# Kernel optimization log

Measured on AMD Instinct MI355X. Metric: run time of the kernel, lower is better.

Reference implementation:

```python
import jax, jax.numpy as jnp
import numpy as np

B, P, D, H = 2048, 128, 64, 8
DB = 10  # D_obs + D_pos = 7 + 3, hard-coded in the module


def setup_inputs() -> dict:
    key = jax.random.key(0)
    ks = jax.random.split(key, 10)
    s = lambda fan_in: 1.0 / np.sqrt(fan_in)
    return {
        "x": jax.random.normal(ks[0], (B, D), dtype=jnp.float32),
        "b": jax.random.normal(ks[1], (B, P, DB), dtype=jnp.float32),
        "W_kvx": jax.random.uniform(ks[2], (D, 2 * H * D), jnp.float32, -s(D), s(D)),
        "b_kvx": jax.random.uniform(ks[3], (2 * H * D,), jnp.float32, -s(D), s(D)),
        "W_kvb": jax.random.uniform(ks[4], (DB, 2 * H * D), jnp.float32, -s(DB), s(DB)),
        "b_kvb": jax.random.uniform(ks[5], (2 * H * D,), jnp.float32, -s(DB), s(DB)),
        "W_q": jax.random.uniform(ks[6], (D, H * D), jnp.float32, -s(D), s(D)),
        "b_q": jax.random.uniform(ks[7], (H * D,), jnp.float32, -s(D), s(D)),
        "W_f": jax.random.uniform(ks[8], (H * D, D), jnp.float32, -s(H * D), s(H * D)),
        "b_f": jax.random.uniform(ks[9], (D,), jnp.float32, -s(H * D), s(H * D)),
    }


def reference(x, b, W_kvx, b_kvx, W_kvb, b_kvb, W_q, b_q, W_f, b_f):
    Bn, Dx = x.shape
    _, Pn, _ = b.shape
    # dual projections + broadcast add: [B,1,2HD] + [B,P,2HD]
    kv = (x @ W_kvx + b_kvx)[:, None, :] + (jnp.einsum('bpe,ef->bpf', b, W_kvb) + b_kvb)
    k, v = jnp.split(kv, 2, axis=-1)            # each [B,P,H*D]
    k = k.reshape(Bn, Pn, H, Dx)
    v = v.reshape(Bn, Pn, H, Dx)
    q = (x @ W_q + b_q).reshape(Bn, H, Dx)
    dots = jnp.einsum('bphd,bhd->bph', k, q) / np.sqrt(Dx).astype(np.float32)
    # NOTE: faithful to source — softmax over the HEAD axis (last dim of [B,P,H])
    attn = jax.nn.softmax(dots, axis=-1)
    vals = jnp.einsum('bph,bphd->bhd', attn, v)  # sum over positions P
    out = vals.reshape(Bn, H * Dx) @ W_f + b_f
    return out
```

## Files before the change

### kernel.cpp

```cpp
#include <hip/hip_runtime.h>

#define NDB 10

__global__ __launch_bounds__(256) void proj_kernel(
    const float* __restrict__ x, const float* __restrict__ W_kvx,
    const float* __restrict__ b_kvx, const float* __restrict__ b_kvb,
    const float* __restrict__ W_q, const float* __restrict__ b_q,
    float* __restrict__ XQ)
{
    __shared__ float x_t[64][68];
    const int t = threadIdx.x;
    const int row0 = blockIdx.x * 64;
    const int ct = blockIdx.y;

    {
        const int r = t & 63, kb = (t >> 6) * 16;
        float4 xv[4];
        #pragma unroll
        for (int i = 0; i < 4; ++i)
            xv[i] = *(const float4*)&x[(size_t)(row0 + r) * 64 + kb + i * 4];
        #pragma unroll
        for (int i = 0; i < 4; ++i) {
            x_t[kb + i * 4 + 0][r] = xv[i].x;
            x_t[kb + i * 4 + 1][r] = xv[i].y;
            x_t[kb + i * 4 + 2][r] = xv[i].z;
            x_t[kb + i * 4 + 3][r] = xv[i].w;
        }
    }
    __syncthreads();

    const bool iskv = (ct < 16);
    const int c0 = (iskv ? ct * 64 : (ct - 16) * 64) + (t & 15) * 4;
    const int stride = iskv ? 1024 : 512;
    const float* Wp = (iskv ? W_kvx : W_q) + c0;
    const int r0 = (t >> 4) * 4;

    float acc[4][4] = {};
    #pragma unroll 8
    for (int k = 0; k < 64; ++k) {
        float4 a  = *(const float4*)&x_t[k][r0];
        float4 wv = *(const float4*)&Wp[k * stride];
        float av[4] = {a.x, a.y, a.z, a.w};
        float wvv[4] = {wv.x, wv.y, wv.z, wv.w};
        #pragma unroll
        for (int i = 0; i < 4; ++i)
            #pragma unroll
            for (int jj = 0; jj < 4; ++jj)
                acc[i][jj] = fmaf(av[i], wvv[jj], acc[i][jj]);
    }
    float4 bias;
    if (iskv) {
        float4 b1 = *(const float4*)&b_kvx[c0];
        float4 b2 = *(const float4*)&b_kvb[c0];
        bias.x = b1.x + b2.x; bias.y = b1.y + b2.y;
        bias.z = b1.z + b2.z; bias.w = b1.w + b2.w;
    } else {
        bias = *(const float4*)&b_q[c0];
    }
    const int outcol = ct * 64 + (t & 15) * 4;
    #pragma unroll
    for (int i = 0; i < 4; ++i) {
        float4 o;
        o.x = acc[i][0] + bias.x; o.y = acc[i][1] + bias.y;
        o.z = acc[i][2] + bias.z; o.w = acc[i][3] + bias.w;
        *(float4*)&XQ[(size_t)(row0 + r0 + i) * 1536 + outcol] = o;
    }
}

__global__ __launch_bounds__(256) void attn_core(
    const float* __restrict__ bmat, const float* __restrict__ W_kvb,
    const float* __restrict__ XQ, const float* __restrict__ W_f,
    const float* __restrict__ b_f, float* __restrict__ out)
{
    __shared__ float bb_s[128][11];
    __shared__ float q_s[8][68];
    __shared__ float dot0_s[8];
    __shared__ float Wqkb_s[NDB][8];
    __shared__ float partA[4][8];
    __shared__ float partS[4][NDB][8];
    __shared__ float A_s[8];
    __shared__ float S_s[NDB][8];
    __shared__ float vals_s[512];
    __shared__ float pout[4][64];

    const int t = threadIdx.x, lane = t & 63, w = t >> 6;
    const int row = blockIdx.x;
    const float* __restrict__ xq = XQ + (size_t)row * 1536;

    {
        const float* bsrc = bmat + (size_t)row * 1280;
        #pragma unroll
        for (int i = 0; i < 5; ++i) {
            int idx = t + 256 * i;
            bb_s[idx / 10][idx % 10] = bsrc[idx];
        }
        float qa = xq[1024 + t];
        float qb = xq[1024 + 256 + t];
        q_s[t >> 6][t & 63] = qa;
        q_s[(t + 256) >> 6][t & 63] = qb;
        float p1 = xq[t] * qa;
        float p2 = xq[t + 256] * qb;
        #pragma unroll
        for (int m = 1; m <= 32; m <<= 1) p1 += __shfl_xor(p1, m);
        #pragma unroll
        for (int m = 1; m <= 32; m <<= 1) p2 += __shfl_xor(p2, m);
        if (lane == 0) { dot0_s[w] = p1; dot0_s[w + 4] = p2; }
    }
    __syncthreads();

    {
        const int g = t >> 3, l = t & 7;
        #pragma unroll
        for (int ro = 0; ro < 3; ++ro) {
            int o = g + 32 * ro;
            if (o < 80) {
                int e = o >> 3, h = o & 7;
                float s = 0.f;
                #pragma unroll
                for (int m = 0; m < 8; ++m) {
                    int d = l + 8 * m;
                    s = fmaf(W_kvb[e * 1024 + h * 64 + d], q_s[h][d], s);
                }
                s += __shfl_xor(s, 1); s += __shfl_xor(s, 2); s += __shfl_xor(s, 4);
                if (l == 0) Wqkb_s[e][h] = s;
            }
        }
    }
    __syncthreads();

    {
        const int hh = lane & 7, pg = lane >> 3;
        float wq[NDB];
        #pragma unroll
        for (int e = 0; e < NDB; ++e) wq[e] = Wqkb_s[e][hh];
        const float d0v = dot0_s[hh];
        float aA = 0.f, aS[NDB];
        #pragma unroll
        for (int e = 0; e < NDB; ++e) aS[e] = 0.f;
        #pragma unroll
        for (int it = 0; it < 4; ++it) {
            int p = w * 32 + pg + 8 * it;
            float bbv[NDB];
            #pragma unroll
            for (int e = 0; e < NDB; ++e) bbv[e] = bb_s[p][e];
            float dot = d0v;
            #pragma unroll
            for (int e = 0; e < NDB; ++e) dot = fmaf(bbv[e], wq[e], dot);
            dot *= 0.125f;
            float m = dot;
            m = fmaxf(m, __shfl_xor(m, 1));
            m = fmaxf(m, __shfl_xor(m, 2));
            m = fmaxf(m, __shfl_xor(m, 4));
            float ex = __expf(dot - m);
            float sum = ex;
            sum += __shfl_xor(sum, 1); sum += __shfl_xor(sum, 2); sum += __shfl_xor(sum, 4);
            float at = ex * __builtin_amdgcn_rcpf(sum);
            aA += at;
            #pragma unroll
            for (int e = 0; e < NDB; ++e) aS[e] = fmaf(at, bbv[e], aS[e]);
        }
        aA += __shfl_xor(aA, 8); aA += __shfl_xor(aA, 16); aA += __shfl_xor(aA, 32);
        #pragma unroll
        for (int e = 0; e < NDB; ++e) {
            aS[e] += __shfl_xor(aS[e], 8);
            aS[e] += __shfl_xor(aS[e], 16);
            aS[e] += __shfl_xor(aS[e], 32);
        }
        if (pg == 0) {
            partA[w][hh] = aA;
            #pragma unroll
            for (int e = 0; e < NDB; ++e) partS[w][e][hh] = aS[e];
        }
    }
    __syncthreads();

    if (t < 8)  A_s[t] = partA[0][t] + partA[1][t] + partA[2][t] + partA[3][t];
    if (t < 80) {
        int e = t >> 3, h = t & 7;
        S_s[e][h] = partS[0][e][h] + partS[1][e][h] + partS[2][e][h] + partS[3][e][h];
    }
    __syncthreads();

    {
        int f1 = t, f2 = t + 256;
        float v1 = A_s[w] * xq[512 + f1];
        float v2 = A_s[w + 4] * xq[512 + f2];
        #pragma unroll
        for (int e = 0; e < NDB; ++e) {
            v1 = fmaf(S_s[e][w],     W_kvb[e * 1024 + 512 + f1], v1);
            v2 = fmaf(S_s[e][w + 4], W_kvb[e * 1024 + 512 + f2], v2);
        }
        vals_s[f1] = v1;
        vals_s[f2] = v2;
    }
    __syncthreads();

    {
        const int j = lane;
        float acc = 0.f;
        #pragma unroll 8
        for (int k4 = 0; k4 < 32; ++k4) {
            int f = w * 128 + k4 * 4;
            float4 v = *(const float4*)&vals_s[f];
            acc = fmaf(v.x, W_f[(f + 0) * 64 + j], acc);
            acc = fmaf(v.y, W_f[(f + 1) * 64 + j], acc);
            acc = fmaf(v.z, W_f[(f + 2) * 64 + j], acc);
            acc = fmaf(v.w, W_f[(f + 3) * 64 + j], acc);
        }
        pout[w][j] = acc;
    }
    __syncthreads();

    if (t < 64)
        out[(size_t)row * 64 + t] =
            pout[0][t] + pout[1][t] + pout[2][t] + pout[3][t] + b_f[t];
}

extern "C" void kernel_launch(void* const* d_in, const int* in_sizes, int n_in,
                              void* d_out, int out_size, void* d_ws, size_t ws_size,
                              hipStream_t stream)
{
    const float* x     = (const float*)d_in[0];
    const float* bmat  = (const float*)d_in[1];
    const float* W_kvx = (const float*)d_in[2];
    const float* b_kvx = (const float*)d_in[3];
    const float* W_kvb = (const float*)d_in[4];
    const float* b_kvb = (const float*)d_in[5];
    const float* W_q   = (const float*)d_in[6];
    const float* b_q   = (const float*)d_in[7];
    const float* W_f   = (const float*)d_in[8];
    const float* b_f   = (const float*)d_in[9];
    float* out = (float*)d_out;
    float* XQ  = (float*)d_ws;

    proj_kernel<<<dim3(32, 24), 256, 0, stream>>>(x, W_kvx, b_kvx, b_kvb, W_q, b_q, XQ);
    attn_core<<<2048, 256, 0, stream>>>(bmat, W_kvb, XQ, W_f, b_f, out);
}
```

Baseline: 109.2 us.

## Fold W_f into value projection weights to skip per-row output GEMV

```diff
diff --git a/kernel.cpp b/kernel.cpp
--- a/kernel.cpp
+++ b/kernel.cpp
@@ -1,12 +1,45 @@
 #include <hip/hip_runtime.h>
 
 #define NDB 10
+
+__global__ __launch_bounds__(256) void fold_kernel(
+    const float* __restrict__ W_kvx, const float* __restrict__ b_kvx,
+    const float* __restrict__ W_kvb, const float* __restrict__ b_kvb,
+    const float* __restrict__ W_f, float* __restrict__ M,
+    float* __restrict__ c, float* __restrict__ T)
+{
+    const int r = blockIdx.x;
+    const int col = blockIdx.y * 256 + threadIdx.x;
+    const int h = col >> 6, j = col & 63;
+
+    const float* wfp = W_f + (size_t)(h * 64) * 64 + j;
+    float acc = 0.f;
+    if (r < 64) {
+        const float* src = W_kvx + (size_t)r * 1024 + 512 + h * 64;
+        #pragma unroll 8
+        for (int d = 0; d < 64; ++d) acc = fmaf(src[d], wfp[d * 64], acc);
+        M[(size_t)r * 512 + col] = acc;
+    } else if (r < 74) {
+        const int e = r - 64;
+        const float* src = W_kvb + (size_t)e * 1024 + 512 + h * 64;
+        #pragma unroll 8
+        for (int d = 0; d < 64; ++d) acc = fmaf(src[d], wfp[d * 64], acc);
+        T[(size_t)e * 512 + col] = acc;
+    } else {
+        const float* s1 = b_kvx + 512 + h * 64;
+        const float* s2 = b_kvb + 512 + h * 64;
+        #pragma unroll 8
+        for (int d = 0; d < 64; ++d) acc = fmaf(s1[d] + s2[d], wfp[d * 64], acc);
+        c[col] = acc;
+    }
+}
 
 __global__ __launch_bounds__(256) void proj_kernel(
     const float* __restrict__ x, const float* __restrict__ W_kvx,
     const float* __restrict__ b_kvx, const float* __restrict__ b_kvb,
     const float* __restrict__ W_q, const float* __restrict__ b_q,
-    float* __restrict__ XQ)
+    const float* __restrict__ M, const float* __restrict__ c,
+    float* __restrict__ XU)
 {
     __shared__ float x_t[64][68];
     const int t = threadIdx.x;
@@ -29,10 +62,12 @@
     }
     __syncthreads();
 
-    const bool iskv = (ct < 16);
-    const int c0 = (iskv ? ct * 64 : (ct - 16) * 64) + (t & 15) * 4;
-    const int stride = iskv ? 1024 : 512;
-    const float* Wp = (iskv ? W_kvx : W_q) + c0;
+    const int cc = (t & 15) * 4;
+    const float* Wp; int stride, c0;
+    if (ct < 8)       { Wp = W_kvx; stride = 1024; c0 = ct * 64 + cc; }
+    else if (ct < 16) { Wp = W_q;   stride = 512;  c0 = (ct - 8) * 64 + cc; }
+    else              { Wp = M;     stride = 512;  c0 = (ct - 16) * 64 + cc; }
+    Wp += c0;
     const int r0 = (t >> 4) * 4;
 
     float acc[4][4] = {};
@@ -49,27 +84,29 @@
                 acc[i][jj] = fmaf(av[i], wvv[jj], acc[i][jj]);
     }
     float4 bias;
-    if (iskv) {
+    if (ct < 8) {
         float4 b1 = *(const float4*)&b_kvx[c0];
         float4 b2 = *(const float4*)&b_kvb[c0];
         bias.x = b1.x + b2.x; bias.y = b1.y + b2.y;
         bias.z = b1.z + b2.z; bias.w = b1.w + b2.w;
+    } else if (ct < 16) {
+        bias = *(const float4*)&b_q[c0];
     } else {
-        bias = *(const float4*)&b_q[c0];
-    }
-    const int outcol = ct * 64 + (t & 15) * 4;
+        bias = *(const float4*)&c[c0];
+    }
+    const int outcol = ct * 64 + cc;
     #pragma unroll
     for (int i = 0; i < 4; ++i) {
         float4 o;
         o.x = acc[i][0] + bias.x; o.y = acc[i][1] + bias.y;
         o.z = acc[i][2] + bias.z; o.w = acc[i][3] + bias.w;
-        *(float4*)&XQ[(size_t)(row0 + r0 + i) * 1536 + outcol] = o;
+        *(float4*)&XU[(size_t)(row0 + r0 + i) * 1536 + outcol] = o;
     }
 }
 
 __global__ __launch_bounds__(256) void attn_core(
     const float* __restrict__ bmat, const float* __restrict__ W_kvb,
-    const float* __restrict__ XQ, const float* __restrict__ W_f,
+    const float* __restrict__ XU, const float* __restrict__ T,
     const float* __restrict__ b_f, float* __restrict__ out)
 {
     __shared__ float bb_s[128][11];
@@ -80,12 +117,11 @@
     __shared__ float partS[4][NDB][8];
     __shared__ float A_s[8];
     __shared__ float S_s[NDB][8];
-    __shared__ float vals_s[512];
     __shared__ float pout[4][64];
 
     const int t = threadIdx.x, lane = t & 63, w = t >> 6;
     const int row = blockIdx.x;
-    const float* __restrict__ xq = XQ + (size_t)row * 1536;
+    const float* __restrict__ xq = XU + (size_t)row * 1536;
 
     {
         const float* bsrc = bmat + (size_t)row * 1280;
@@ -94,8 +130,8 @@
             int idx = t + 256 * i;
             bb_s[idx / 10][idx % 10] = bsrc[idx];
         }
-        float qa = xq[1024 + t];
-        float qb = xq[1024 + 256 + t];
+        float qa = xq[512 + t];
+        float qb = xq[512 + 256 + t];
         q_s[t >> 6][t & 63] = qa;
         q_s[(t + 256) >> 6][t & 63] = qb;
         float p1 = xq[t] * qa;
@@ -182,30 +218,15 @@
     __syncthreads();
 
     {
-        int f1 = t, f2 = t + 256;
-        float v1 = A_s[w] * xq[512 + f1];
-        float v2 = A_s[w + 4] * xq[512 + f2];
-        #pragma unroll
-        for (int e = 0; e < NDB; ++e) {
-            v1 = fmaf(S_s[e][w],     W_kvb[e * 1024 + 512 + f1], v1);
-            v2 = fmaf(S_s[e][w + 4], W_kvb[e * 1024 + 512 + f2], v2);
-        }
-        vals_s[f1] = v1;
-        vals_s[f2] = v2;
-    }
-    __syncthreads();
-
-    {
         const int j = lane;
         float acc = 0.f;
-        #pragma unroll 8
-        for (int k4 = 0; k4 < 32; ++k4) {
-            int f = w * 128 + k4 * 4;
-            float4 v = *(const float4*)&vals_s[f];
-            acc = fmaf(v.x, W_f[(f + 0) * 64 + j], acc);
-            acc = fmaf(v.y, W_f[(f + 1) * 64 + j], acc);
-            acc = fmaf(v.z, W_f[(f + 2) * 64 + j], acc);
-            acc = fmaf(v.w, W_f[(f + 3) * 64 + j], acc);
+        #pragma unroll
+        for (int hi = 0; hi < 2; ++hi) {
+            int h = 2 * w + hi;
+            acc = fmaf(A_s[h], xq[1024 + h * 64 + j], acc);
+            #pragma unroll
+            for (int e = 0; e < NDB; ++e)
+                acc = fmaf(S_s[e][h], T[e * 512 + h * 64 + j], acc);
         }
         pout[w][j] = acc;
     }
@@ -231,8 +252,13 @@
     const float* W_f   = (const float*)d_in[8];
     const float* b_f   = (const float*)d_in[9];
     float* out = (float*)d_out;
-    float* XQ  = (float*)d_ws;
-
-    proj_kernel<<<dim3(32, 24), 256, 0, stream>>>(x, W_kvx, b_kvx, b_kvb, W_q, b_q, XQ);
-    attn_core<<<2048, 256, 0, stream>>>(bmat, W_kvb, XQ, W_f, b_f, out);
-}
+
+    float* XU = (float*)d_ws;
+    float* M  = XU + (size_t)2048 * 1536;
+    float* c  = M + 64 * 512;
+    float* T  = c + 512;
+
+    fold_kernel<<<dim3(75, 2), 256, 0, stream>>>(W_kvx, b_kvx, W_kvb, b_kvb, W_f, M, c, T);
+    proj_kernel<<<dim3(32, 24), 256, 0, stream>>>(x, W_kvx, b_kvx, b_kvb, W_q, b_q, M, c, XU);
+    attn_core<<<2048, 256, 0, stream>>>(bmat, W_kvb, XU, T, b_f, out);
+}
```

Measured after the change: 106.7 us. 2.2% less time.
